# Kernel tuning notes

Hardware: AMD Instinct MI355X
Metric: run time of the kernel (lower is better)

The kernel has to match this reference:

```python
import jax, jax.numpy as jnp
import numpy as np

N_HEADS = 8
D_HEAD = 64


def setup_inputs() -> dict:
    key = jax.random.key(0)
    ks = jax.random.split(key, 7)
    B, Sq, Dm = 16, 4096, 512
    Skv, Dc = 77, 768
    inner = N_HEADS * D_HEAD  # 512
    s = lambda d: 1.0 / np.sqrt(d)
    return {
        "x": jax.random.normal(ks[0], (B, Sq, Dm), jnp.float32),
        "context": jax.random.normal(ks[1], (B, Skv, Dc), jnp.float32),
        "Wq": jax.random.normal(ks[2], (Dm, inner), jnp.float32) * s(Dm),
        "Wk": jax.random.normal(ks[3], (Dc, inner), jnp.float32) * s(Dc),
        "Wv": jax.random.normal(ks[4], (Dc, inner), jnp.float32) * s(Dc),
        "Wout": jax.random.normal(ks[5], (inner, inner), jnp.float32) * s(inner),
        "bout": jnp.zeros((inner,), jnp.float32),
    }


def reference(x, context, Wq, Wk, Wv, Wout, bout):
    B, Sq, _ = x.shape
    Skv = context.shape[1]
    scale = D_HEAD ** (-0.5)
    # projections (no bias)
    q = (x @ Wq).reshape(B, Sq, N_HEADS, D_HEAD)
    k = (context @ Wk).reshape(B, Skv, N_HEADS, D_HEAD)
    v = (context @ Wv).reshape(B, Skv, N_HEADS, D_HEAD)
    # scores: [B, H, Sq, Skv]
    score = jnp.einsum("bqhd,bkhd->bhqk", q, k) * scale
    weights = jax.nn.softmax(score, axis=-1)
    attn = jnp.einsum("bhqk,bkhd->bqhd", weights, v)
    h = attn.reshape(B, Sq, N_HEADS * D_HEAD)
    return h @ Wout + bout
```

## Files before the change

### kernel.cpp

```cpp
#include <hip/hip_runtime.h>


typedef unsigned short u16;
typedef unsigned int u32;
typedef _Float16 f16;
typedef __attribute__((ext_vector_type(8))) _Float16 half8;
typedef __attribute__((ext_vector_type(4))) _Float16 half4;
typedef __attribute__((ext_vector_type(4))) float f32x4;

__device__ __forceinline__ f32x4 mfma16h(half8 a, half8 b, f32x4 c) {
    return __builtin_amdgcn_mfma_f32_16x16x32_f16(a, b, c, 0, 0, 0);
}
__device__ __forceinline__ void gl_lds16(const f16* g, f16* l) {
    __builtin_amdgcn_global_load_lds(
        (const __attribute__((address_space(1))) void*)g,
        (__attribute__((address_space(3))) void*)l, 16, 0, 0);
}

__global__ __launch_bounds__(256) void pad_fill(
    f16* __restrict__ vT, f16* __restrict__ kbuf)
{
    const int nv = 16 * 512 * 19;
    int i = blockIdx.x * 256 + threadIdx.x;
    if (i < nv) {
        int g = i / 19, s = i - g * 19;
        vT[(size_t)g * 96 + 77 + s] = (f16)0.f;
    } else {
        int j = i - nv;
        if (j < 8 * 512) kbuf[(size_t)1232 * 512 + j] = (f16)0.f;
    }
}

__global__ __launch_bounds__(256) void transpose4(
    const float* __restrict__ Wq, const float* __restrict__ Wk,
    const float* __restrict__ Wv, const float* __restrict__ Wo,
    f16* __restrict__ WqT, f16* __restrict__ WkT,
    f16* __restrict__ WvT, f16* __restrict__ WoT)
{
    int idx = blockIdx.x * 256 + threadIdx.x;
    const float* W; f16* T; int K; int base;
    if (idx < 262144)        { W = Wq; T = WqT; K = 512; base = 0; }
    else if (idx < 655360)   { W = Wk; T = WkT; K = 768; base = 262144; }
    else if (idx < 1048576)  { W = Wv; T = WvT; K = 768; base = 655360; }
    else if (idx < 1310720)  { W = Wo; T = WoT; K = 512; base = 1048576; }
    else return;
    int j = idx - base;
    int n = j / K, k = j - n * K;
    T[j] = (f16)W[(size_t)k * 512 + n];
}

__global__ __launch_bounds__(256) void gemm_kv(
    const float* __restrict__ A, const f16* __restrict__ Bt,
    f16* __restrict__ kbuf, f16* __restrict__ vT)
{
    __shared__ f16 lA[64 * 40];
    __shared__ f16 lB[64 * 40];

    const int t = threadIdx.x;
    const int lane = t & 63;
    const int w = t >> 6;
    const int wr = w >> 1, wc = w & 1;
    const int m0 = blockIdx.x * 64, n0 = blockIdx.y * 64;
    const int ar = lane & 15;
    const int kc = (lane >> 4) << 3;

    const int srow = t >> 2;
    const int sc8  = (t & 3) << 3;

    f32x4 acc[2][2] = {};

    for (int k0 = 0; k0 < 768; k0 += 32) {
        float4 v0 = make_float4(0.f, 0.f, 0.f, 0.f);
        float4 v1 = make_float4(0.f, 0.f, 0.f, 0.f);
        int gr = m0 + srow;
        if (gr < 1232) {
            v0 = *(const float4*)(A + (size_t)gr * 768 + k0 + sc8);
            v1 = *(const float4*)(A + (size_t)gr * 768 + k0 + sc8 + 4);
        }
        half8 ha = {(f16)v0.x, (f16)v0.y, (f16)v0.z, (f16)v0.w,
                    (f16)v1.x, (f16)v1.y, (f16)v1.z, (f16)v1.w};
        *(half8*)(lA + srow * 40 + sc8) = ha;
        *(half8*)(lB + srow * 40 + sc8) =
            *(const half8*)(Bt + (size_t)(n0 + srow) * 768 + k0 + sc8);
        __syncthreads();

        half8 fa[2], fb[2];
        #pragma unroll
        for (int m = 0; m < 2; ++m)
            fa[m] = *(const half8*)(lA + (wr * 32 + m * 16 + ar) * 40 + kc);
        #pragma unroll
        for (int n = 0; n < 2; ++n)
            fb[n] = *(const half8*)(lB + (wc * 32 + n * 16 + ar) * 40 + kc);
        #pragma unroll
        for (int m = 0; m < 2; ++m)
            #pragma unroll
            for (int n = 0; n < 2; ++n)
                acc[m][n] = mfma16h(fa[m], fb[n], acc[m][n]);
        __syncthreads();
    }

    #pragma unroll
    for (int n = 0; n < 2; ++n) {
        int col = n0 + wc * 32 + n * 16 + ar;
        #pragma unroll
        for (int m = 0; m < 2; ++m) {
            #pragma unroll
            for (int r = 0; r < 4; ++r) {
                int row = m0 + wr * 32 + m * 16 + ((lane >> 4) << 2) + r;
                if (row < 1232) {
                    f16 v = (f16)acc[m][n][r];
                    if (col < 512) {
                        kbuf[(size_t)row * 512 + col] = v;
                    } else {
                        int bb = row / 77;
                        int si = row - bb * 77;
                        vT[((size_t)bb * 512 + (col - 512)) * 96 + si] = v;
                    }
                }
            }
        }
    }
}

__global__ __launch_bounds__(256, 2) void gemm_x16(
    const float* __restrict__ A, const f16* __restrict__ B,
    f16* __restrict__ CHalf, int M, int N, int K)
{
    __shared__ f16 sA[2][128 * 32];
    __shared__ f16 sB[2][256 * 32];

    const int t = threadIdx.x;
    const int lane = t & 63;
    const int w = t >> 6;
    const int wr = w >> 1, wc = w & 1;

    const int f = blockIdx.x + gridDim.x * blockIdx.y;
    const int cpx = (gridDim.x * gridDim.y) >> 3;
    const int logical = (f & 7) * cpx + (f >> 3);
    const int m0 = (logical / gridDim.x) * 128;
    const int n0 = (logical % gridDim.x) * 256;

    const int ar = lane & 15;
    const int kc = (lane >> 4) << 3;

    const int arow = t >> 1;
    const int acol = (t & 1) << 4;
    const int brow = lane >> 2;
    const int bcol = (lane & 3) << 3;

    f32x4 acc[4][8] = {};
    f32x4 rA[4];

    auto LOAD_A = [&](int kt) {
        const float* p = A + (size_t)(m0 + arow) * K + (kt << 5) + acol;
        #pragma unroll
        for (int j = 0; j < 4; ++j) rA[j] = *(const f32x4*)(p + j * 4);
    };
    auto WRITE_A = [&](int buf) {
        half8 h0 = { (f16)rA[0].x, (f16)rA[0].y, (f16)rA[0].z, (f16)rA[0].w,
                     (f16)rA[1].x, (f16)rA[1].y, (f16)rA[1].z, (f16)rA[1].w };
        half8 h1 = { (f16)rA[2].x, (f16)rA[2].y, (f16)rA[2].z, (f16)rA[2].w,
                     (f16)rA[3].x, (f16)rA[3].y, (f16)rA[3].z, (f16)rA[3].w };
        *(half8*)(&sA[buf][arow * 32 + acol])     = h0;
        *(half8*)(&sA[buf][arow * 32 + acol + 8]) = h1;
    };
    auto STAGE_B = [&](int buf, int kt) {
        #pragma unroll
        for (int j = 0; j < 4; ++j) {
            const int ci = w * 4 + j;
            gl_lds16(B + (size_t)(n0 + ci * 16 + brow) * K + (kt << 5) + bcol,
                     &sB[buf][ci * 512]);
        }
    };

    const int nk = K >> 5;
    LOAD_A(0);
    STAGE_B(0, 0);
    WRITE_A(0);
    __syncthreads();

    int cur = 0;
    for (int kt = 0; kt < nk; ++kt) {
        if (kt + 1 < nk) {
            LOAD_A(kt + 1);
            STAGE_B(cur ^ 1, kt + 1);
        }

        half8 fa[4], fb[8];
        #pragma unroll
        for (int m = 0; m < 4; ++m)
            fa[m] = *(const half8*)(&sA[cur][(wr * 64 + m * 16 + ar) * 32 + kc]);
        #pragma unroll
        for (int n = 0; n < 8; ++n)
            fb[n] = *(const half8*)(&sB[cur][(wc * 128 + n * 16 + ar) * 32 + kc]);

        __builtin_amdgcn_s_setprio(1);
        #pragma unroll
        for (int m = 0; m < 4; ++m)
            #pragma unroll
            for (int n = 0; n < 8; ++n)
                acc[m][n] = mfma16h(fa[m], fb[n], acc[m][n]);
        __builtin_amdgcn_s_setprio(0);

        if (kt + 1 < nk) WRITE_A(cur ^ 1);
        __syncthreads();
        cur ^= 1;
    }

    #pragma unroll
    for (int n = 0; n < 8; ++n) {
        int col = n0 + wc * 128 + n * 16 + ar;
        #pragma unroll
        for (int m = 0; m < 4; ++m) {
            #pragma unroll
            for (int r = 0; r < 4; ++r) {
                int row = m0 + wr * 64 + m * 16 + ((lane >> 4) << 2) + r;
                CHalf[(size_t)row * N + col] = (f16)acc[m][n][r];
            }
        }
    }
}

__global__ __launch_bounds__(256, 2) void gemm_h16(
    const f16* __restrict__ A, const f16* __restrict__ B,
    const float* __restrict__ bias, float* __restrict__ C,
    int M, int N, int K)
{
    __shared__ f16 sA[2][128 * 32];
    __shared__ f16 sB[2][256 * 32];

    const int t = threadIdx.x;
    const int lane = t & 63;
    const int w = t >> 6;
    const int wr = w >> 1, wc = w & 1;

    const int f = blockIdx.x + gridDim.x * blockIdx.y;
    const int cpx = (gridDim.x * gridDim.y) >> 3;
    const int logical = (f & 7) * cpx + (f >> 3);
    const int m0 = (logical / gridDim.x) * 128;
    const int n0 = (logical % gridDim.x) * 256;

    const int ar = lane & 15;
    const int kc = (lane >> 4) << 3;
    const int srow = lane >> 2;
    const int scol = (lane & 3) << 3;

    f32x4 acc[4][8] = {};

    auto STAGE = [&](int buf, int kt) {
        #pragma unroll
        for (int j = 0; j < 2; ++j) {
            const int ci = w * 2 + j;
            gl_lds16(A + (size_t)(m0 + ci * 16 + srow) * K + (kt << 5) + scol,
                     &sA[buf][ci * 512]);
        }
        #pragma unroll
        for (int j = 0; j < 4; ++j) {
            const int ci = w * 4 + j;
            gl_lds16(B + (size_t)(n0 + ci * 16 + srow) * K + (kt << 5) + scol,
                     &sB[buf][ci * 512]);
        }
    };

    const int nk = K >> 5;
    STAGE(0, 0);
    __syncthreads();

    int cur = 0;
    for (int kt = 0; kt < nk; ++kt) {
        if (kt + 1 < nk) STAGE(cur ^ 1, kt + 1);

        half8 fa[4], fb[8];
        #pragma unroll
        for (int m = 0; m < 4; ++m)
            fa[m] = *(const half8*)(&sA[cur][(wr * 64 + m * 16 + ar) * 32 + kc]);
        #pragma unroll
        for (int n = 0; n < 8; ++n)
            fb[n] = *(const half8*)(&sB[cur][(wc * 128 + n * 16 + ar) * 32 + kc]);

        __builtin_amdgcn_s_setprio(1);
        #pragma unroll
        for (int m = 0; m < 4; ++m)
            #pragma unroll
            for (int n = 0; n < 8; ++n)
                acc[m][n] = mfma16h(fa[m], fb[n], acc[m][n]);
        __builtin_amdgcn_s_setprio(0);
        __syncthreads();
        cur ^= 1;
    }

    #pragma unroll
    for (int n = 0; n < 8; ++n) {
        int col = n0 + wc * 128 + n * 16 + ar;
        float bv = bias[col];
        #pragma unroll
        for (int m = 0; m < 4; ++m) {
            #pragma unroll
            for (int r = 0; r < 4; ++r) {
                int row = m0 + wr * 64 + m * 16 + ((lane >> 4) << 2) + r;
                C[(size_t)row * N + col] = acc[m][n][r] + bv;
            }
        }
    }
}

__global__ __launch_bounds__(256) void attn_h16(
    const f16* __restrict__ q, const f16* __restrict__ k,
    const f16* __restrict__ vT, f16* __restrict__ outA)
{
    constexpr int PST = 104;
    __shared__ f16 sP[4 * 32 * PST];

    const int t = threadIdx.x;
    const int lane = t & 63;
    const int w = t >> 6;
    const int ar = lane & 15;
    const int kg = lane >> 4;
    const int kc = kg << 3;
    const int b = blockIdx.z, head = blockIdx.y;
    const size_t qrow0 = (size_t)b * 4096 + blockIdx.x * 128 + w * 32;

    f32x4 accs[2][5] = {};
    #pragma unroll
    for (int ks = 0; ks < 2; ++ks) {
        const int d = head * 64 + ks * 32 + kc;
        half8 ah[2];
        #pragma unroll
        for (int m = 0; m < 2; ++m)
            ah[m] = *(const half8*)(q + (qrow0 + m * 16 + ar) * 512 + d);
        #pragma unroll
        for (int n = 0; n < 5; ++n) {
            half8 bh = *(const half8*)(k + ((size_t)(b * 77 + n * 16 + ar)) * 512 + d);
            #pragma unroll
            for (int m = 0; m < 2; ++m)
                accs[m][n] = mfma16h(ah[m], bh, accs[m][n]);
        }
    }

    #pragma unroll
    for (int m = 0; m < 2; ++m) {
        #pragma unroll
        for (int r = 0; r < 4; ++r) {
            float mx = -1e30f;
            #pragma unroll
            for (int n = 0; n < 5; ++n) {
                float v = accs[m][n][r] * 0.125f;
                if (n == 4 && ar >= 13) v = -1e30f;
                accs[m][n][r] = v;
                mx = fmaxf(mx, v);
            }
            mx = fmaxf(mx, __shfl_xor(mx, 1));
            mx = fmaxf(mx, __shfl_xor(mx, 2));
            mx = fmaxf(mx, __shfl_xor(mx, 4));
            mx = fmaxf(mx, __shfl_xor(mx, 8));
            float sum = 0.f;
            #pragma unroll
            for (int n = 0; n < 5; ++n) {
                float e = __expf(accs[m][n][r] - mx);
                accs[m][n][r] = e;
                sum += e;
            }
            sum += __shfl_xor(sum, 1);
            sum += __shfl_xor(sum, 2);
            sum += __shfl_xor(sum, 4);
            sum += __shfl_xor(sum, 8);
            float inv = 1.f / sum;
            #pragma unroll
            for (int n = 0; n < 5; ++n) accs[m][n][r] *= inv;
        }
    }

    f16* myP = sP + w * 32 * PST;
    for (int i = lane; i < 32 * 12; i += 64) {
        int row = i / 12, c = 80 + (i % 12) * 2;
        *(u32*)(myP + row * PST + c) = 0;
    }
    #pragma unroll
    for (int m = 0; m < 2; ++m)
        #pragma unroll
        for (int n = 0; n < 5; ++n)
            #pragma unroll
            for (int r = 0; r < 4; ++r)
                myP[(m * 16 + kg * 4 + r) * PST + n * 16 + ar] = (f16)accs[m][n][r];

    f32x4 accp[2][4] = {};
    #pragma unroll
    for (int ks = 0; ks < 3; ++ks) {
        half8 pa[2];
        #pragma unroll
        for (int m = 0; m < 2; ++m)
            pa[m] = *(const half8*)(myP + (m * 16 + ar) * PST + ks * 32 + kc);
        #pragma unroll
        for (int n = 0; n < 4; ++n) {
            half8 bh = *(const half8*)(vT + ((size_t)b * 512 + head * 64 + n * 16 + ar) * 96 + ks * 32 + kc);
            #pragma unroll
            for (int m = 0; m < 2; ++m)
                accp[m][n] = mfma16h(pa[m], bh, accp[m][n]);
        }
    }

    #pragma unroll
    for (int m = 0; m < 2; ++m)
        #pragma unroll
        for (int n = 0; n < 4; ++n)
            #pragma unroll
            for (int r = 0; r < 4; ++r)
                outA[(qrow0 + m * 16 + kg * 4 + r) * 512 + head * 64 + n * 16 + ar]
                    = (f16)accp[m][n][r];
}

extern "C" void kernel_launch(void* const* d_in, const int* in_sizes, int n_in,
                              void* d_out, int out_size, void* d_ws, size_t ws_size,
                              hipStream_t stream)
{
    const float* x    = (const float*)d_in[0];
    const float* ctx  = (const float*)d_in[1];
    const float* Wq   = (const float*)d_in[2];
    const float* Wk   = (const float*)d_in[3];
    const float* Wv   = (const float*)d_in[4];
    const float* Wout = (const float*)d_in[5];
    const float* bout = (const float*)d_in[6];

    char* ws = (char*)d_ws;
    size_t off = 0;
    auto alloc = [&](size_t bytes) -> void* {
        void* p = ws + off;
        off += (bytes + 255) & ~(size_t)255;
        return p;
    };
    f16* WqT = (f16*)alloc(512 * 512 * 2);
    f16* WkT = (f16*)alloc(768 * 512 * 2);
    f16* WvT = (f16*)alloc(768 * 512 * 2);
    f16* WoT = (f16*)alloc(512 * 512 * 2);
    f16* kbuf = (f16*)alloc((size_t)1240 * 512 * 2);
    f16* vT   = (f16*)alloc((size_t)16 * 512 * 96 * 2);
    f16* qh   = (f16*)alloc((size_t)65536 * 512 * 2);
    f16* attnA = (f16*)alloc((size_t)65536 * 512 * 2);
    (void)ws_size; (void)in_sizes; (void)n_in; (void)out_size;

    pad_fill<<<dim3(625), dim3(256), 0, stream>>>(vT, kbuf);

    transpose4<<<dim3(5120), dim3(256), 0, stream>>>(
        Wq, Wk, Wv, Wout, WqT, WkT, WvT, WoT);

    gemm_kv<<<dim3(20, 16), dim3(256), 0, stream>>>(ctx, WkT, kbuf, vT);

    gemm_x16<<<dim3(2, 512), dim3(256), 0, stream>>>(
        x, WqT, qh, 65536, 512, 512);

    attn_h16<<<dim3(32, 8, 16), dim3(256), 0, stream>>>(qh, kbuf, vT, attnA);

    gemm_h16<<<dim3(2, 512), dim3(256), 0, stream>>>(
        attnA, WoT, bout, (float*)d_out, 65536, 512, 512);
}
```

Baseline: 223.4 us.

## Rewrite output-projection GEMM as 8-wave 256x256 tile with phased prefetch

Replaces the output-projection GEMM with a 512-thread kernel that computes 256x256 tiles using a K-step of 64. Each K-tile is split into four phases that interleave MFMA work with staged global-to-LDS loads, and the LDS layout is XOR-swizzled. A and B are prefetched one and two tiles ahead, synchronised with explicit vmcnt waits and barriers. The goal is to raise data reuse per block and hide load latency. The cost is more LDS and registers per block and lower occupancy.

```diff
diff --git a/kernel.cpp b/kernel.cpp
--- a/kernel.cpp
+++ b/kernel.cpp
@@ -221,83 +221,126 @@
     }
 }
 
-__global__ __launch_bounds__(256, 2) void gemm_h16(
+__global__ __launch_bounds__(512) void gemm_h16_8p(
     const f16* __restrict__ A, const f16* __restrict__ B,
     const float* __restrict__ bias, float* __restrict__ C,
     int M, int N, int K)
 {
-    __shared__ f16 sA[2][128 * 32];
-    __shared__ f16 sB[2][256 * 32];
+    __shared__ f16 sA[2][2][128 * 64];
+    __shared__ f16 sB[2][2][128 * 64];
 
     const int t = threadIdx.x;
     const int lane = t & 63;
     const int w = t >> 6;
-    const int wr = w >> 1, wc = w & 1;
+    const int wr = w >> 2;
+    const int wc = w & 3;
 
     const int f = blockIdx.x + gridDim.x * blockIdx.y;
     const int cpx = (gridDim.x * gridDim.y) >> 3;
     const int logical = (f & 7) * cpx + (f >> 3);
-    const int m0 = (logical / gridDim.x) * 128;
+    const int m0 = (logical / gridDim.x) * 256;
     const int n0 = (logical % gridDim.x) * 256;
 
     const int ar = lane & 15;
-    const int kc = (lane >> 4) << 3;
-    const int srow = lane >> 2;
-    const int scol = (lane & 3) << 3;
-
-    f32x4 acc[4][8] = {};
-
-    auto STAGE = [&](int buf, int kt) {
+    const int kg = lane >> 4;
+    const int kc = kg << 3;
+    const int swz = (ar & 4) ? 16 : 0;
+
+    const int srow = lane >> 3;
+    const int scol = ((lane & 7) << 3) ^ ((lane >= 32) ? 16 : 0);
+
+    f32x4 acc[8][4] = {};
+
+    auto STAGE_A = [&](int tile, int h) {
+        const int kb = tile << 6;
         #pragma unroll
         for (int j = 0; j < 2; ++j) {
-            const int ci = w * 2 + j;
-            gl_lds16(A + (size_t)(m0 + ci * 16 + srow) * K + (kt << 5) + scol,
-                     &sA[buf][ci * 512]);
-        }
-        #pragma unroll
-        for (int j = 0; j < 4; ++j) {
-            const int ci = w * 4 + j;
-            gl_lds16(B + (size_t)(n0 + ci * 16 + srow) * K + (kt << 5) + scol,
-                     &sB[buf][ci * 512]);
-        }
-    };
-
-    const int nk = K >> 5;
-    STAGE(0, 0);
-    __syncthreads();
-
-    int cur = 0;
-    for (int kt = 0; kt < nk; ++kt) {
-        if (kt + 1 < nk) STAGE(cur ^ 1, kt + 1);
-
-        half8 fa[4], fb[8];
-        #pragma unroll
-        for (int m = 0; m < 4; ++m)
-            fa[m] = *(const half8*)(&sA[cur][(wr * 64 + m * 16 + ar) * 32 + kc]);
-        #pragma unroll
-        for (int n = 0; n < 8; ++n)
-            fb[n] = *(const half8*)(&sB[cur][(wc * 128 + n * 16 + ar) * 32 + kc]);
-
-        __builtin_amdgcn_s_setprio(1);
-        #pragma unroll
-        for (int m = 0; m < 4; ++m)
-            #pragma unroll
-            for (int n = 0; n < 8; ++n)
-                acc[m][n] = mfma16h(fa[m], fb[n], acc[m][n]);
-        __builtin_amdgcn_s_setprio(0);
-        __syncthreads();
-        cur ^= 1;
-    }
-
-    #pragma unroll
-    for (int n = 0; n < 8; ++n) {
-        int col = n0 + wc * 128 + n * 16 + ar;
-        float bv = bias[col];
-        #pragma unroll
-        for (int m = 0; m < 4; ++m) {
+            const int c = w * 2 + j;
+            gl_lds16(A + (size_t)(m0 + h * 128 + c * 8 + srow) * K + kb + scol,
+                     &sA[tile & 1][h][c * 512]);
+        }
+    };
+    auto STAGE_B = [&](int tile, int h) {
+        const int kb = tile << 6;
+        #pragma unroll
+        for (int j = 0; j < 2; ++j) {
+            const int c = w * 2 + j;
+            gl_lds16(B + (size_t)(n0 + h * 128 + c * 8 + srow) * K + kb + scol,
+                     &sB[tile & 1][h][c * 512]);
+        }
+    };
+
+    const int nk = K >> 6;
+
+    STAGE_A(0, 0); STAGE_A(0, 1);
+    STAGE_B(0, 0); STAGE_B(0, 1);
+    STAGE_B(1, 0); STAGE_B(1, 1);
+    asm volatile("s_waitcnt vmcnt(4)" ::: "memory");
+    __builtin_amdgcn_sched_barrier(0);
+    __builtin_amdgcn_s_barrier();
+    __builtin_amdgcn_sched_barrier(0);
+
+    #pragma unroll 1
+    for (int T = 0; T < nk; ++T) {
+        const f16* pA = &sA[T & 1][wr][0];
+        const f16* pB = &sB[T & 1][wc >> 1][0];
+        const int brow0 = (wc & 1) * 64;
+        half8 fb[4][2];
+
+        #pragma unroll
+        for (int q = 0; q < 4; ++q) {
+            if (q == 0) {
+                #pragma unroll
+                for (int n = 0; n < 4; ++n)
+                    #pragma unroll
+                    for (int ks = 0; ks < 2; ++ks)
+                        fb[n][ks] = *(const half8*)(pB + (brow0 + n * 16 + ar) * 64
+                                                       + ((ks * 32 + kc) ^ swz));
+            }
+            half8 fa[2][2];
+            #pragma unroll
+            for (int j = 0; j < 2; ++j)
+                #pragma unroll
+                for (int ks = 0; ks < 2; ++ks)
+                    fa[j][ks] = *(const half8*)(pA + ((q * 2 + j) * 16 + ar) * 64
+                                                   + ((ks * 32 + kc) ^ swz));
+
+            if (q == 0)      { if (T + 1 < nk) STAGE_A(T + 1, 0); }
+            else if (q == 1) { if (T + 1 < nk) STAGE_A(T + 1, 1); }
+            else if (q == 2) { if (T + 2 < nk) STAGE_B(T + 2, 0); }
+            else             { if (T + 2 < nk) STAGE_B(T + 2, 1); }
+
+            __builtin_amdgcn_s_barrier();
+            __builtin_amdgcn_s_setprio(1);
+            #pragma unroll
+            for (int j = 0; j < 2; ++j)
+                #pragma unroll
+                for (int n = 0; n < 4; ++n)
+                    #pragma unroll
+                    for (int ks = 0; ks < 2; ++ks)
+                        acc[q * 2 + j][n] =
+                            mfma16h(fa[j][ks], fb[n][ks], acc[q * 2 + j][n]);
+            __builtin_amdgcn_s_setprio(0);
+
+            if (q == 3) {
+                if (T + 2 < nk) asm volatile("s_waitcnt vmcnt(4)" ::: "memory");
+                else            asm volatile("s_waitcnt vmcnt(0)" ::: "memory");
+                __builtin_amdgcn_sched_barrier(0);
+            }
+            __builtin_amdgcn_s_barrier();
+            __builtin_amdgcn_sched_barrier(0);
+        }
+    }
+
+    #pragma unroll
+    for (int n = 0; n < 4; ++n) {
+        const int col = n0 + wc * 64 + n * 16 + ar;
+        const float bv = bias[col];
+        #pragma unroll
+        for (int m = 0; m < 8; ++m) {
             #pragma unroll
             for (int r = 0; r < 4; ++r) {
-                int row = m0 + wr * 64 + m * 16 + ((lane >> 4) << 2) + r;
+                const int row = m0 + wr * 128 + m * 16 + kg * 4 + r;
                 C[(size_t)row * N + col] = acc[m][n][r] + bv;
             }
         }
@@ -450,6 +493,6 @@
 
     attn_h16<<<dim3(32, 8, 16), dim3(256), 0, stream>>>(qh, kbuf, vT, attnA);
 
-    gemm_h16<<<dim3(2, 512), dim3(256), 0, stream>>>(
+    gemm_h16_8p<<<dim3(2, 256), dim3(512), 0, stream>>>(
         attnA, WoT, bout, (float*)d_out, 65536, 512, 512);
 }
```

Measured after the change: 227.9 us. 1.02x slower.

## Enlarge Q/output GEMM tiles to 256x256 with 8 waves; merge prep kernels

Applied to the files above, without the earlier changes.

Both large projection GEMMs move from 128x256 tiles with 4 waves to 256x256 tiles with 512 threads (8 waves in a 2x4 arrangement), each wave computing 128x64. Each block now does twice the work per B tile, which halves the B traffic per output and halves the grid. The pad-fill and weight-transpose kernels are merged into one launch to remove a kernel launch. Occupancy drops to one block per CU, and LDS use grows to 64KB per block, which may reduce latency hiding.

```diff
diff --git a/kernel.cpp b/kernel.cpp
--- a/kernel.cpp
+++ b/kernel.cpp
@@ -17,11 +17,27 @@
         (__attribute__((address_space(3))) void*)l, 16, 0, 0);
 }
 
-__global__ __launch_bounds__(256) void pad_fill(
+__global__ __launch_bounds__(256) void prep(
+    const float* __restrict__ Wq, const float* __restrict__ Wk,
+    const float* __restrict__ Wv, const float* __restrict__ Wo,
+    f16* __restrict__ WqT, f16* __restrict__ WkT,
+    f16* __restrict__ WvT, f16* __restrict__ WoT,
     f16* __restrict__ vT, f16* __restrict__ kbuf)
 {
+    int idx = blockIdx.x * 256 + threadIdx.x;
+    if (idx < 1310720) {
+        const float* W; f16* T; int K; int base;
+        if (idx < 262144)        { W = Wq; T = WqT; K = 512; base = 0; }
+        else if (idx < 655360)   { W = Wk; T = WkT; K = 768; base = 262144; }
+        else if (idx < 1048576)  { W = Wv; T = WvT; K = 768; base = 655360; }
+        else                     { W = Wo; T = WoT; K = 512; base = 1048576; }
+        int j = idx - base;
+        int n = j / K, k = j - n * K;
+        T[j] = (f16)W[(size_t)k * 512 + n];
+        return;
+    }
+    int i = idx - 1310720;
     const int nv = 16 * 512 * 19;
-    int i = blockIdx.x * 256 + threadIdx.x;
     if (i < nv) {
         int g = i / 19, s = i - g * 19;
         vT[(size_t)g * 96 + 77 + s] = (f16)0.f;
@@ -29,24 +45,6 @@
         int j = i - nv;
         if (j < 8 * 512) kbuf[(size_t)1232 * 512 + j] = (f16)0.f;
     }
-}
-
-__global__ __launch_bounds__(256) void transpose4(
-    const float* __restrict__ Wq, const float* __restrict__ Wk,
-    const float* __restrict__ Wv, const float* __restrict__ Wo,
-    f16* __restrict__ WqT, f16* __restrict__ WkT,
-    f16* __restrict__ WvT, f16* __restrict__ WoT)
-{
-    int idx = blockIdx.x * 256 + threadIdx.x;
-    const float* W; f16* T; int K; int base;
-    if (idx < 262144)        { W = Wq; T = WqT; K = 512; base = 0; }
-    else if (idx < 655360)   { W = Wk; T = WkT; K = 768; base = 262144; }
-    else if (idx < 1048576)  { W = Wv; T = WvT; K = 768; base = 655360; }
-    else if (idx < 1310720)  { W = Wo; T = WoT; K = 512; base = 1048576; }
-    else return;
-    int j = idx - base;
-    int n = j / K, k = j - n * K;
-    T[j] = (f16)W[(size_t)k * 512 + n];
 }
 
 __global__ __launch_bounds__(256) void gemm_kv(
@@ -122,33 +120,35 @@
     }
 }
 
-__global__ __launch_bounds__(256, 2) void gemm_x16(
+__global__ __launch_bounds__(512, 1) void gemm_x16(
     const float* __restrict__ A, const f16* __restrict__ B,
     f16* __restrict__ CHalf, int M, int N, int K)
 {
-    __shared__ f16 sA[2][128 * 32];
+    __shared__ f16 sA[2][256 * 32];
     __shared__ f16 sB[2][256 * 32];
 
     const int t = threadIdx.x;
     const int lane = t & 63;
     const int w = t >> 6;
-    const int wr = w >> 1, wc = w & 1;
+    const int wr = w >> 2;
+    const int wc = w & 3;
 
     const int f = blockIdx.x + gridDim.x * blockIdx.y;
     const int cpx = (gridDim.x * gridDim.y) >> 3;
     const int logical = (f & 7) * cpx + (f >> 3);
-    const int m0 = (logical / gridDim.x) * 128;
+    const int m0 = (logical / gridDim.x) * 256;
     const int n0 = (logical % gridDim.x) * 256;
 
     const int ar = lane & 15;
-    const int kc = (lane >> 4) << 3;
+    const int kg = lane >> 4;
+    const int kc = kg << 3;
 
     const int arow = t >> 1;
     const int acol = (t & 1) << 4;
     const int brow = lane >> 2;
     const int bcol = (lane & 3) << 3;
 
-    f32x4 acc[4][8] = {};
+    f32x4 acc[8][4] = {};
     f32x4 rA[4];
 
     auto LOAD_A = [&](int kt) {
@@ -166,8 +166,8 @@
     };
     auto STAGE_B = [&](int buf, int kt) {
         #pragma unroll
-        for (int j = 0; j < 4; ++j) {
-            const int ci = w * 4 + j;
+        for (int j = 0; j < 2; ++j) {
+            const int ci = w * 2 + j;
             gl_lds16(B + (size_t)(n0 + ci * 16 + brow) * K + (kt << 5) + bcol,
                      &sB[buf][ci * 512]);
         }
@@ -186,19 +186,19 @@
             STAGE_B(cur ^ 1, kt + 1);
         }
 
-        half8 fa[4], fb[8];
-        #pragma unroll
-        for (int m = 0; m < 4; ++m)
-            fa[m] = *(const half8*)(&sA[cur][(wr * 64 + m * 16 + ar) * 32 + kc]);
-        #pragma unroll
-        for (int n = 0; n < 8; ++n)
-            fb[n] = *(const half8*)(&sB[cur][(wc * 128 + n * 16 + ar) * 32 + kc]);
+        half8 fa[8], fb[4];
+        #pragma unroll
+        for (int m = 0; m < 8; ++m)
+            fa[m] = *(const half8*)(&sA[cur][(wr * 128 + m * 16 + ar) * 32 + kc]);
+        #pragma unroll
+        for (int n = 0; n < 4; ++n)
+            fb[n] = *(const half8*)(&sB[cur][(wc * 64 + n * 16 + ar) * 32 + kc]);
 
         __builtin_amdgcn_s_setprio(1);
         #pragma unroll
-        for (int m = 0; m < 4; ++m)
-            #pragma unroll
-            for (int n = 0; n < 8; ++n)
+        for (int m = 0; m < 8; ++m)
+            #pragma unroll
+            for (int n = 0; n < 4; ++n)
                 acc[m][n] = mfma16h(fa[m], fb[n], acc[m][n]);
         __builtin_amdgcn_s_setprio(0);
 
@@ -208,44 +208,46 @@
     }
 
     #pragma unroll
-    for (int n = 0; n < 8; ++n) {
-        int col = n0 + wc * 128 + n * 16 + ar;
-        #pragma unroll
-        for (int m = 0; m < 4; ++m) {
+    for (int n = 0; n < 4; ++n) {
+        int col = n0 + wc * 64 + n * 16 + ar;
+        #pragma unroll
+        for (int m = 0; m < 8; ++m) {
             #pragma unroll
             for (int r = 0; r < 4; ++r) {
-                int row = m0 + wr * 64 + m * 16 + ((lane >> 4) << 2) + r;
+                int row = m0 + wr * 128 + m * 16 + kg * 4 + r;
                 CHalf[(size_t)row * N + col] = (f16)acc[m][n][r];
             }
         }
     }
 }
 
-__global__ __launch_bounds__(256, 2) void gemm_h16(
+__global__ __launch_bounds__(512, 1) void gemm_h16(
     const f16* __restrict__ A, const f16* __restrict__ B,
     const float* __restrict__ bias, float* __restrict__ C,
     int M, int N, int K)
 {
-    __shared__ f16 sA[2][128 * 32];
+    __shared__ f16 sA[2][256 * 32];
     __shared__ f16 sB[2][256 * 32];
 
     const int t = threadIdx.x;
     const int lane = t & 63;
     const int w = t >> 6;
-    const int wr = w >> 1, wc = w & 1;
+    const int wr = w >> 2;
+    const int wc = w & 3;
 
     const int f = blockIdx.x + gridDim.x * blockIdx.y;
     const int cpx = (gridDim.x * gridDim.y) >> 3;
     const int logical = (f & 7) * cpx + (f >> 3);
-    const int m0 = (logical / gridDim.x) * 128;
+    const int m0 = (logical / gridDim.x) * 256;
     const int n0 = (logical % gridDim.x) * 256;
 
     const int ar = lane & 15;
-    const int kc = (lane >> 4) << 3;
+    const int kg = lane >> 4;
+    const int kc = kg << 3;
     const int srow = lane >> 2;
     const int scol = (lane & 3) << 3;
 
-    f32x4 acc[4][8] = {};
+    f32x4 acc[8][4] = {};
 
     auto STAGE = [&](int buf, int kt) {
         #pragma unroll
@@ -255,8 +257,8 @@
                      &sA[buf][ci * 512]);
         }
         #pragma unroll
-        for (int j = 0; j < 4; ++j) {
-            const int ci = w * 4 + j;
+        for (int j = 0; j < 2; ++j) {
+            const int ci = w * 2 + j;
             gl_lds16(B + (size_t)(n0 + ci * 16 + srow) * K + (kt << 5) + scol,
                      &sB[buf][ci * 512]);
         }
@@ -270,19 +272,19 @@
     for (int kt = 0; kt < nk; ++kt) {
         if (kt + 1 < nk) STAGE(cur ^ 1, kt + 1);
 
-        half8 fa[4], fb[8];
-        #pragma unroll
-        for (int m = 0; m < 4; ++m)
-            fa[m] = *(const half8*)(&sA[cur][(wr * 64 + m * 16 + ar) * 32 + kc]);
-        #pragma unroll
-        for (int n = 0; n < 8; ++n)
-            fb[n] = *(const half8*)(&sB[cur][(wc * 128 + n * 16 + ar) * 32 + kc]);
+        half8 fa[8], fb[4];
+        #pragma unroll
+        for (int m = 0; m < 8; ++m)
+            fa[m] = *(const half8*)(&sA[cur][(wr * 128 + m * 16 + ar) * 32 + kc]);
+        #pragma unroll
+        for (int n = 0; n < 4; ++n)
+            fb[n] = *(const half8*)(&sB[cur][(wc * 64 + n * 16 + ar) * 32 + kc]);
 
         __builtin_amdgcn_s_setprio(1);
         #pragma unroll
-        for (int m = 0; m < 4; ++m)
-            #pragma unroll
-            for (int n = 0; n < 8; ++n)
+        for (int m = 0; m < 8; ++m)
+            #pragma unroll
+            for (int n = 0; n < 4; ++n)
                 acc[m][n] = mfma16h(fa[m], fb[n], acc[m][n]);
         __builtin_amdgcn_s_setprio(0);
         __syncthreads();
@@ -290,14 +292,14 @@
     }
 
     #pragma unroll
-    for (int n = 0; n < 8; ++n) {
-        int col = n0 + wc * 128 + n * 16 + ar;
+    for (int n = 0; n < 4; ++n) {
+        int col = n0 + wc * 64 + n * 16 + ar;
         float bv = bias[col];
         #pragma unroll
-        for (int m = 0; m < 4; ++m) {
+        for (int m = 0; m < 8; ++m) {
             #pragma unroll
             for (int r = 0; r < 4; ++r) {
-                int row = m0 + wr * 64 + m * 16 + ((lane >> 4) << 2) + r;
+                int row = m0 + wr * 128 + m * 16 + kg * 4 + r;
                 C[(size_t)row * N + col] = acc[m][n][r] + bv;
             }
         }
@@ -438,18 +440,16 @@
     f16* attnA = (f16*)alloc((size_t)65536 * 512 * 2);
     (void)ws_size; (void)in_sizes; (void)n_in; (void)out_size;
 
-    pad_fill<<<dim3(625), dim3(256), 0, stream>>>(vT, kbuf);
-
-    transpose4<<<dim3(5120), dim3(256), 0, stream>>>(
-        Wq, Wk, Wv, Wout, WqT, WkT, WvT, WoT);
+    prep<<<dim3(5744), dim3(256), 0, stream>>>(
+        Wq, Wk, Wv, Wout, WqT, WkT, WvT, WoT, vT, kbuf);
 
     gemm_kv<<<dim3(20, 16), dim3(256), 0, stream>>>(ctx, WkT, kbuf, vT);
 
-    gemm_x16<<<dim3(2, 512), dim3(256), 0, stream>>>(
+    gemm_x16<<<dim3(2, 256), dim3(512), 0, stream>>>(
         x, WqT, qh, 65536, 512, 512);
 
     attn_h16<<<dim3(32, 8, 16), dim3(256), 0, stream>>>(qh, kbuf, vT, attnA);
 
-    gemm_h16<<<dim3(2, 512), dim3(256), 0, stream>>>(
+    gemm_h16<<<dim3(2, 256), dim3(512), 0, stream>>>(
         attnA, WoT, bout, (float*)d_out, 65536, 512, 512);
 }
```

Result: slower. 240.9 us (+7.9%).
